# Kernel tuning notes

Hardware: AMD Instinct MI355X
Metric: run time of the kernel (lower is better)

The kernel has to match this reference:

```python
import jax, jax.numpy as jnp
import numpy as np


def setup_inputs() -> dict:
    key = jax.random.key(0)
    ks = jax.random.split(key, 5)
    B, S, E, H = 2, 2048, 1024, 16
    scale = 1.0 / np.sqrt(E)
    return {
        "input": jax.random.normal(ks[0], (B, S, E), dtype=jnp.float32),
        "Wqkv": jax.random.normal(ks[1], (3 * E, E), dtype=jnp.float32) * scale,
        "bqkv": jax.random.normal(ks[2], (3 * E,), dtype=jnp.float32) * 0.01,
        "Wo": jax.random.normal(ks[3], (E, E), dtype=jnp.float32) * scale,
        "bo": jax.random.normal(ks[4], (E,), dtype=jnp.float32) * 0.01,
    }


def reference(input, Wqkv, bqkv, Wo, bo):
    H = 16
    B, S, E = input.shape
    dh = E // H
    # fused QKV projection: [B, S, 3E]
    qkv = input @ Wqkv.T + bqkv
    qkv = qkv.reshape(B, S, 3, H, dh)
    qkv = jnp.transpose(qkv, (2, 0, 3, 1, 4))  # [3, B, H, S, dh]
    q, k, v = qkv[0], qkv[1], qkv[2]
    # scores [B, H, Sq, Sk]
    scores = jnp.einsum("bhqd,bhkd->bhqk", q, k) / jnp.sqrt(jnp.float32(dh))
    # NOTE: original code softmaxes over dim=2 (the QUERY axis) — reproduced faithfully
    attn = jax.nn.softmax(scores, axis=2)
    out = jnp.einsum("bhqk,bhkd->bhqd", attn, v)  # [B, H, S, dh]
    out = jnp.transpose(out, (0, 2, 1, 3)).reshape(B, S, E)
    return out @ Wo.T + bo
```

## Files before the change

kernel.cpp:

```cpp
#include <hip/hip_runtime.h>
#include <math.h>

#define B_ 2
#define S_ 2048
#define E_ 1024
#define H_ 16
#define DH_ 64
#define NE3_ 3072
#define MTOT_ (B_*S_)
#define QSCALE_ 0.18033688011112042f

typedef __bf16 bf16;
typedef bf16 bf16x8 __attribute__((ext_vector_type(8)));
typedef bf16 bf16x4 __attribute__((ext_vector_type(4)));
typedef float f32x4 __attribute__((ext_vector_type(4)));

#define MFMA16(a,b,c) __builtin_amdgcn_mfma_f32_16x16x32_bf16(a,b,c,0,0,0)

#define F_(r) ((((r) & 7) ^ (((r) >> 3) & 7)))

__device__ inline void* lds_swz(void* base, int row, int bytecol) {
    return (char*)base + row * 128 + (bytecol ^ (F_(row) << 4));
}

__device__ inline unsigned cvt_pk_bf16(float lo, float hi) {
    unsigned r;
    asm("v_cvt_pk_bf16_f32 %0, %1, %2" : "=v"(r) : "v"(lo), "v"(hi));
    return r;
}

__device__ inline float exp2_hw(float x) {
    float r;
    asm("v_exp_f32 %0, %1" : "=v"(r) : "v"(x));
    return r;
}

__device__ inline void gload_lds16(const void* g, void* l) {
    __builtin_amdgcn_global_load_lds(
        (const __attribute__((address_space(1))) void*)g,
        (__attribute__((address_space(3))) void*)l, 16, 0, 0);
}

#define NX_ (MTOT_*E_)
#define NW_ (NE3_*E_)
#define NWO_ (E_*E_)
__global__ void k_f2b3(const float* __restrict__ x, const float* __restrict__ wq,
                       const float* __restrict__ wo,
                       bf16* __restrict__ xb, bf16* __restrict__ wqb,
                       bf16* __restrict__ wob) {
    const int i = blockIdx.x * 256 + threadIdx.x;
    const int idx = i * 4;
    const float* src; bf16* dst; int off;
    if (idx < NX_)            { src = x;  dst = xb;  off = idx; }
    else if (idx < NX_ + NW_) { src = wq; dst = wqb; off = idx - NX_; }
    else                      { src = wo; dst = wob; off = idx - NX_ - NW_; }
    float4 f = *reinterpret_cast<const float4*>(src + off);
    bf16x4 o;
    o[0] = (bf16)f.x; o[1] = (bf16)f.y; o[2] = (bf16)f.z; o[3] = (bf16)f.w;
    *reinterpret_cast<bf16x4*>(dst + off) = o;
}

template<int MODE>
__global__ __launch_bounds__(256) void k_gemm(
    const bf16* __restrict__ A, const bf16* __restrict__ W,
    const float* __restrict__ bias,
    bf16* __restrict__ Qb, bf16* __restrict__ Kb, bf16* __restrict__ Vt,
    float* __restrict__ out)
{
    __shared__ __align__(16) bf16 At[2][128*64];
    __shared__ __align__(16) bf16 Bt[2][128*64];
    const int tid = threadIdx.x, lane = tid & 63, w = tid >> 6;
    const int wr = w >> 1, wc = w & 1;
    const int g = blockIdx.x;
    const int nxw = (MODE == 0 ? 3 : 1);
    const int xcd = g & 7, li = g >> 3;
    const int m0 = (li & 31) * 128;
    const int n0 = (xcd * nxw + (li >> 5)) * 128;

    f32x4 acc[4][4] = {};
    const int lrow = lane >> 3, lcol = (lane & 7) * 8;

    auto stage = [&](int k0, int buf) {
        for (int c4 = 0; c4 < 4; ++c4) {
            const int c = w * 4 + c4;
            const int row = c * 8 + lrow;
            const int colx = lcol ^ (F_(row) * 8);
            gload_lds16(A + (size_t)(m0 + row) * E_ + k0 + colx, &At[buf][c * 512]);
            gload_lds16(W + (size_t)(n0 + row) * E_ + k0 + colx, &Bt[buf][c * 512]);
        }
    };
    stage(0, 0);
    __syncthreads();

    int cur = 0;
    for (int kt = 0; kt < E_/64; ++kt) {
        if (kt + 1 < E_/64) stage((kt + 1) * 64, cur ^ 1);
        for (int ks = 0; ks < 2; ++ks) {
            const int bc = ks * 64 + 16 * (lane >> 4);
            bf16x8 a[4], b[4];
            for (int j = 0; j < 4; ++j)
                a[j] = *(const bf16x8*)lds_swz(&At[cur][0], wr*64 + j*16 + (lane&15), bc);
            for (int i = 0; i < 4; ++i)
                b[i] = *(const bf16x8*)lds_swz(&Bt[cur][0], wc*64 + i*16 + (lane&15), bc);
            for (int i = 0; i < 4; ++i)
                for (int j = 0; j < 4; ++j)
                    acc[i][j] = MFMA16(b[i], a[j], acc[i][j]);
        }
        cur ^= 1;
        if (kt + 1 < E_/64) __syncthreads();
    }

    const int mW = m0 + wr*64;
    for (int i = 0; i < 4; ++i) {
        const int n4 = n0 + wc*64 + i*16 + (lane >> 4) * 4;
        const float4 b4 = *reinterpret_cast<const float4*>(&bias[n4]);
        const float* bp = reinterpret_cast<const float*>(&b4);
        if constexpr (MODE == 0) {
            const int t = n4 >> 10, h = (n4 >> 6) & 15, d0 = n4 & 63;
            for (int j = 0; j < 4; ++j) {
                const int m = mW + j*16 + (lane & 15);
                const int bb_i = m >> 11, s = m & 2047;
                if (t == 2) {
                    for (int r = 0; r < 4; ++r)
                        Vt[(((size_t)(bb_i*H_ + h))*DH_ + d0 + r)*S_ + s] =
                            (bf16)(acc[i][j][r] + bp[r]);
                } else {
                    bf16* dst = (t == 0) ? Qb : Kb;
                    const float sc = (t == 0) ? QSCALE_ : 1.0f;
                    bf16x4 o;
                    for (int r = 0; r < 4; ++r)
                        o[r] = (bf16)((acc[i][j][r] + bp[r]) * sc);
                    *reinterpret_cast<bf16x4*>(
                        dst + (((size_t)(bb_i*H_ + h))*S_ + s)*DH_ + d0) = o;
                }
            }
        } else {
            for (int j = 0; j < 4; ++j) {
                const int m = mW + j*16 + (lane & 15);
                float4 o;
                o.x = acc[i][j][0] + bp[0];
                o.y = acc[i][j][1] + bp[1];
                o.z = acc[i][j][2] + bp[2];
                o.w = acc[i][j][3] + bp[3];
                *reinterpret_cast<float4*>(out + (size_t)m * E_ + n4) = o;
            }
        }
    }
}

__global__ __launch_bounds__(256) void k_colsum(
    const bf16* __restrict__ Qb, const bf16* __restrict__ Kb,
    bf16* __restrict__ Vt)
{
    __shared__ __align__(16) bf16 Kl[128*64];
    __shared__ __align__(16) bf16 Ql[2][128*64];
    __shared__ float rlbuf[128];
    const int tid = threadIdx.x, lane = tid & 63, w = tid >> 6;
    const int g = blockIdx.x, xcd = g & 7, li = g >> 3;
    const int bh = xcd * 4 + (li >> 4);
    const int k0 = (li & 15) * 128;
    const bf16* Kbase = Kb + ((size_t)bh * S_ + k0) * DH_;
    const bf16* Qbase = Qb + (size_t)bh * S_ * DH_;

    for (int j = 0; j < 4; ++j) {
        const int idx = j*256 + tid, row = idx >> 3;
        const int colx = ((idx & 7) * 8) ^ (F_(row) * 8);
        gload_lds16(Kbase + (size_t)row * DH_ + colx, &Kl[(j*256 + w*64) * 8]);
    }
    auto stageQ = [&](int qt, int buf) {
        for (int j = 0; j < 4; ++j) {
            const int idx = j*256 + tid, row = idx >> 3;
            const int colx = ((idx & 7) * 8) ^ (F_(row) * 8);
            gload_lds16(Qbase + (size_t)(qt*128 + row) * DH_ + colx,
                        &Ql[buf][(j*256 + w*64) * 8]);
        }
    };
    stageQ(0, 0);
    __syncthreads();

    bf16x8 bk[2][2];
    for (int ks = 0; ks < 2; ++ks) {
        const int bc = ks * 64 + 16 * (lane >> 4);
        bk[ks][0] = *(const bf16x8*)lds_swz(Kl, w*32 + (lane&15), bc);
        bk[ks][1] = *(const bf16x8*)lds_swz(Kl, w*32 + 16 + (lane&15), bc);
    }

    float lsum0 = 0.f, lsum1 = 0.f;
    int cur = 0;
    for (int qt = 0; qt < S_/128; ++qt) {
        if (qt + 1 < S_/128) stageQ(qt + 1, cur ^ 1);
        #pragma unroll
        for (int qi = 0; qi < 8; ++qi) {
            f32x4 s0 = {}, s1 = {};
            for (int ks = 0; ks < 2; ++ks) {
                const int bc = ks * 64 + 16 * (lane >> 4);
                bf16x8 aq = *(const bf16x8*)lds_swz(&Ql[cur][0], qi*16 + (lane&15), bc);
                s0 = MFMA16(aq, bk[ks][0], s0);
                s1 = MFMA16(aq, bk[ks][1], s1);
            }
            for (int r = 0; r < 4; ++r) {
                lsum0 += exp2_hw(s0[r]);
                lsum1 += exp2_hw(s1[r]);
            }
        }
        cur ^= 1;
        if (qt + 1 < S_/128) __syncthreads();
    }
    lsum0 += __shfl_xor(lsum0, 16); lsum0 += __shfl_xor(lsum0, 32);
    lsum1 += __shfl_xor(lsum1, 16); lsum1 += __shfl_xor(lsum1, 32);
    if (lane < 16) {
        rlbuf[w*32 + lane]      = 1.0f / lsum0;
        rlbuf[w*32 + 16 + lane] = 1.0f / lsum1;
    }
    __syncthreads();

    bf16* Vb = Vt + (size_t)bh * DH_ * S_ + k0;
    const int d = tid >> 2, kk = (tid & 3) * 32;
    for (int c = 0; c < 4; ++c) {
        bf16x8* p = reinterpret_cast<bf16x8*>(Vb + (size_t)d * S_ + kk + c*8);
        bf16x8 v = *p, o;
        for (int jj = 0; jj < 8; ++jj)
            o[jj] = (bf16)((float)v[jj] * rlbuf[kk + c*8 + jj]);
        *p = o;
    }
}

__global__ __launch_bounds__(256) void k_attn(
    const bf16* __restrict__ Qb, const bf16* __restrict__ Kb,
    const bf16* __restrict__ Vt, bf16* __restrict__ AO)
{
    __shared__ __align__(16) char smem[49152];
    const int tid = threadIdx.x, lane = tid & 63, w = tid >> 6;
    const int g = blockIdx.x, xcd = g & 7, li = g >> 3;
    const int bh = xcd * 4 + (li >> 4);
    const int q0 = (li & 15) * 128;
    const bf16* Qbase = Qb + ((size_t)bh * S_ + q0) * DH_;
    const bf16* Kbase = Kb + (size_t)bh * S_ * DH_;
    const bf16* Vbase = Vt + (size_t)bh * DH_ * S_;
    char* QP  = smem;
    char* Plw = smem + w * 4096;

    for (int j = 0; j < 4; ++j) {
        const int idx = j*256 + tid, row = idx >> 3;
        const int colx = ((idx & 7) * 8) ^ (F_(row) * 8);
        gload_lds16(Qbase + (size_t)row * DH_ + colx, QP + (j*256 + w*64) * 16);
    }
    auto stageKV = [&](int kt, int buf) {
        for (int j = 0; j < 2; ++j) {
            const int idx = j*256 + tid, row = idx >> 3;
            const int colx = ((idx & 7) * 8) ^ (F_(row) * 8);
            gload_lds16(Kbase + (size_t)(kt*64 + row) * DH_ + colx,
                        smem + 16384 + buf*8192 + (j*256 + w*64) * 16);
            gload_lds16(Vbase + (size_t)row * S_ + kt*64 + colx,
                        smem + 32768 + buf*8192 + (j*256 + w*64) * 16);
        }
    };
    stageKV(0, 0);
    __syncthreads();

    bf16x8 bq[2][2];
    for (int qi = 0; qi < 2; ++qi)
        for (int ks = 0; ks < 2; ++ks)
            bq[qi][ks] = *(const bf16x8*)lds_swz(QP, w*32 + qi*16 + (lane&15),
                                                 ks*64 + 16*(lane>>4));

    f32x4 oacc[4][2] = {};
    int cur = 0;
    for (int kt = 0; kt < S_/64; ++kt) {
        if (kt + 1 < S_/64) stageKV(kt + 1, cur ^ 1);
        char* Kc = smem + 16384 + cur*8192;
        char* Vc = smem + 32768 + cur*8192;

        for (int kf = 0; kf < 4; ++kf) {
            f32x4 sacc[2] = {};
            for (int ks = 0; ks < 2; ++ks) {
                bf16x8 ak = *(const bf16x8*)lds_swz(Kc, kf*16 + (lane&15),
                                                    ks*64 + 16*(lane>>4));
                for (int qi = 0; qi < 2; ++qi)
                    sacc[qi] = MFMA16(ak, bq[qi][ks], sacc[qi]);
            }
            for (int qi = 0; qi < 2; ++qi) {
                uint2 pw;
                pw.x = cvt_pk_bf16(exp2_hw(sacc[qi][0]), exp2_hw(sacc[qi][1]));
                pw.y = cvt_pk_bf16(exp2_hw(sacc[qi][2]), exp2_hw(sacc[qi][3]));
                *(uint2*)lds_swz(Plw, qi*16 + (lane&15), kf*32 + (lane>>4)*8) = pw;
            }
        }

        for (int ks = 0; ks < 2; ++ks) {
            const int bc = ks*64 + 16*(lane>>4);
            bf16x8 av[4], bp[2];
            for (int df = 0; df < 4; ++df)
                av[df] = *(const bf16x8*)lds_swz(Vc, df*16 + (lane&15), bc);
            for (int qi = 0; qi < 2; ++qi)
                bp[qi] = *(const bf16x8*)lds_swz(Plw, qi*16 + (lane&15), bc);
            for (int df = 0; df < 4; ++df)
                for (int qi = 0; qi < 2; ++qi)
                    oacc[df][qi] = MFMA16(av[df], bp[qi], oacc[df][qi]);
        }
        cur ^= 1;
        if (kt + 1 < S_/64) __syncthreads();
    }

    const int b = bh >> 4, h = bh & 15;
    for (int df = 0; df < 4; ++df)
        for (int qi = 0; qi < 2; ++qi) {
            const int d0 = df*16 + (lane >> 4) * 4;
            const int q = q0 + w*32 + qi*16 + (lane & 15);
            bf16x4 o;
            for (int r = 0; r < 4; ++r) o[r] = (bf16)oacc[df][qi][r];
            *reinterpret_cast<bf16x4*>(
                AO + ((size_t)(b*S_ + q))*E_ + h*DH_ + d0) = o;
        }
}

extern "C" void kernel_launch(void* const* d_in, const int* in_sizes, int n_in,
                              void* d_out, int out_size, void* d_ws, size_t ws_size,
                              hipStream_t stream) {
    const float* input = (const float*)d_in[0];
    const float* Wqkv  = (const float*)d_in[1];
    const float* bqkv  = (const float*)d_in[2];
    const float* Wo    = (const float*)d_in[3];
    const float* bo    = (const float*)d_in[4];
    float* out = (float*)d_out;

    char* ws = (char*)d_ws;
    bf16*  Xb   = (bf16*) (ws + 0);
    bf16*  Wqb  = (bf16*) (ws + 8388608);
    bf16*  Wob  = (bf16*) (ws + 14680064);
    bf16*  Qb   = (bf16*) (ws + 16777216);
    bf16*  Kb   = (bf16*) (ws + 25165824);
    bf16*  Vtg  = (bf16*) (ws + 33554432);
    bf16*  AO   = (bf16*) (ws + 41943040);

    k_f2b3<<<(NX_ + NW_ + NWO_) / 1024, 256, 0, stream>>>(
        input, Wqkv, Wo, Xb, Wqb, Wob);

    k_gemm<0><<<768, 256, 0, stream>>>(Xb, Wqb, bqkv, Qb, Kb, Vtg, nullptr);

    k_colsum<<<512, 256, 0, stream>>>(Qb, Kb, Vtg);

    k_attn<<<512, 256, 0, stream>>>(Qb, Kb, Vtg, AO);

    k_gemm<1><<<256, 256, 0, stream>>>(AO, Wob, bo, nullptr, nullptr, nullptr, out);
}
```

Before: 169.2 us.

## Store LDS tiles in MFMA fragment order instead of XOR-swizzled rows

Replaces the XOR-swizzled row-major shared-memory layout with a fragment-major layout. Each 1 KB chunk holds exactly one 16x32 MFMA operand fragment, so every lane reads at a fixed offset of lane*16 with no address arithmetic and no bank conflicts. The global-to-LDS loads are remapped so each wave fills whole fragments, and the P tile in the attention kernel uses a matching layout. The inner loops are also fully unrolled. In exchange, each global load now covers 16 rows by 16 bytes instead of contiguous 128-byte row segments, which can hurt global coalescing.

```diff
diff --git a/kernel.cpp b/kernel.cpp
--- a/kernel.cpp
+++ b/kernel.cpp
@@ -16,12 +16,6 @@
 typedef float f32x4 __attribute__((ext_vector_type(4)));
 
 #define MFMA16(a,b,c) __builtin_amdgcn_mfma_f32_16x16x32_bf16(a,b,c,0,0,0)
-
-#define F_(r) ((((r) & 7) ^ (((r) >> 3) & 7)))
-
-__device__ inline void* lds_swz(void* base, int row, int bytecol) {
-    return (char*)base + row * 128 + (bytecol ^ (F_(row) << 4));
-}
 
 __device__ inline unsigned cvt_pk_bf16(float lo, float hi) {
     unsigned r;
@@ -67,9 +61,12 @@
     bf16* __restrict__ Qb, bf16* __restrict__ Kb, bf16* __restrict__ Vt,
     float* __restrict__ out)
 {
-    __shared__ __align__(16) bf16 At[2][128*64];
-    __shared__ __align__(16) bf16 Bt[2][128*64];
+    __shared__ __align__(16) char smem[65536];
+    char* Abuf = smem;
+    char* Bbuf = smem + 32768;
     const int tid = threadIdx.x, lane = tid & 63, w = tid >> 6;
+    const int lq = lane & 15, lh = lane >> 4;
+    const int l16 = lane * 16;
     const int wr = w >> 1, wc = w & 1;
     const int g = blockIdx.x;
     const int nxw = (MODE == 0 ? 3 : 1);
@@ -77,32 +74,52 @@
     const int m0 = (li & 31) * 128;
     const int n0 = (xcd * nxw + (li >> 5)) * 128;
 
+    const int voffA = lq * E_ + lh * 8;
+
     f32x4 acc[4][4] = {};
-    const int lrow = lane >> 3, lcol = (lane & 7) * 8;
 
     auto stage = [&](int k0, int buf) {
-        for (int c4 = 0; c4 < 4; ++c4) {
-            const int c = w * 4 + c4;
-            const int row = c * 8 + lrow;
-            const int colx = lcol ^ (F_(row) * 8);
-            gload_lds16(A + (size_t)(m0 + row) * E_ + k0 + colx, &At[buf][c * 512]);
-            gload_lds16(W + (size_t)(n0 + row) * E_ + k0 + colx, &Bt[buf][c * 512]);
+        #pragma unroll
+        for (int j = 0; j < 4; ++j) {
+            const int C = j*4 + w;
+            const int rp = (C>>3)*64 + ((C>>1)&3)*16;
+            const int ce = (C&1)*32;
+            gload_lds16(A + (size_t)(m0 + rp) * E_ + k0 + ce + (voffA - lq*E_) + lq*E_,
+                        Abuf + buf*16384 + C*1024);
+            gload_lds16(W + (size_t)(n0 + rp) * E_ + k0 + ce + voffA - lq*E_ + lq*E_,
+                        Bbuf + buf*16384 + C*1024);
         }
     };
-    stage(0, 0);
+    auto stage2 = [&](int k0, int buf) {
+        #pragma unroll
+        for (int j = 0; j < 4; ++j) {
+            const int C = j*4 + w;
+            const int rp = (C>>3)*64 + ((C>>1)&3)*16;
+            const int ce = (C&1)*32;
+            gload_lds16(A + (size_t)(m0 + rp) * E_ + k0 + ce + voffA,
+                        Abuf + buf*16384 + C*1024);
+            gload_lds16(W + (size_t)(n0 + rp) * E_ + k0 + ce + voffA,
+                        Bbuf + buf*16384 + C*1024);
+        }
+    };
+    stage2(0, 0);
     __syncthreads();
 
     int cur = 0;
     for (int kt = 0; kt < E_/64; ++kt) {
-        if (kt + 1 < E_/64) stage((kt + 1) * 64, cur ^ 1);
+        if (kt + 1 < E_/64) stage2((kt + 1) * 64, cur ^ 1);
+        #pragma unroll
         for (int ks = 0; ks < 2; ++ks) {
-            const int bc = ks * 64 + 16 * (lane >> 4);
             bf16x8 a[4], b[4];
+            #pragma unroll
             for (int j = 0; j < 4; ++j)
-                a[j] = *(const bf16x8*)lds_swz(&At[cur][0], wr*64 + j*16 + (lane&15), bc);
+                a[j] = *(const bf16x8*)(Abuf + cur*16384 + (wr*8 + j*2 + ks)*1024 + l16);
+            #pragma unroll
             for (int i = 0; i < 4; ++i)
-                b[i] = *(const bf16x8*)lds_swz(&Bt[cur][0], wc*64 + i*16 + (lane&15), bc);
+                b[i] = *(const bf16x8*)(Bbuf + cur*16384 + (wc*8 + i*2 + ks)*1024 + l16);
+            #pragma unroll
             for (int i = 0; i < 4; ++i)
+                #pragma unroll
                 for (int j = 0; j < 4; ++j)
                     acc[i][j] = MFMA16(b[i], a[j], acc[i][j]);
         }
@@ -112,13 +129,13 @@
 
     const int mW = m0 + wr*64;
     for (int i = 0; i < 4; ++i) {
-        const int n4 = n0 + wc*64 + i*16 + (lane >> 4) * 4;
+        const int n4 = n0 + wc*64 + i*16 + lh * 4;
         const float4 b4 = *reinterpret_cast<const float4*>(&bias[n4]);
         const float* bp = reinterpret_cast<const float*>(&b4);
         if constexpr (MODE == 0) {
             const int t = n4 >> 10, h = (n4 >> 6) & 15, d0 = n4 & 63;
             for (int j = 0; j < 4; ++j) {
-                const int m = mW + j*16 + (lane & 15);
+                const int m = mW + j*16 + lq;
                 const int bb_i = m >> 11, s = m & 2047;
                 if (t == 2) {
                     for (int r = 0; r < 4; ++r)
@@ -136,7 +153,7 @@
             }
         } else {
             for (int j = 0; j < 4; ++j) {
-                const int m = mW + j*16 + (lane & 15);
+                const int m = mW + j*16 + lq;
                 float4 o;
                 o.x = acc[i][j][0] + bp[0];
                 o.y = acc[i][j][1] + bp[1];
@@ -152,38 +169,43 @@
     const bf16* __restrict__ Qb, const bf16* __restrict__ Kb,
     bf16* __restrict__ Vt)
 {
-    __shared__ __align__(16) bf16 Kl[128*64];
-    __shared__ __align__(16) bf16 Ql[2][128*64];
+    __shared__ __align__(16) char smem[49152];
     __shared__ float rlbuf[128];
+    char* Kl   = smem;
+    char* Qbuf = smem + 16384;
     const int tid = threadIdx.x, lane = tid & 63, w = tid >> 6;
+    const int lq = lane & 15, lh = lane >> 4;
+    const int l16 = lane * 16;
     const int g = blockIdx.x, xcd = g & 7, li = g >> 3;
     const int bh = xcd * 4 + (li >> 4);
     const int k0 = (li & 15) * 128;
     const bf16* Kbase = Kb + ((size_t)bh * S_ + k0) * DH_;
     const bf16* Qbase = Qb + (size_t)bh * S_ * DH_;
-
+    const int voffK = lq * DH_ + lh * 8;
+
+    #pragma unroll
     for (int j = 0; j < 4; ++j) {
-        const int idx = j*256 + tid, row = idx >> 3;
-        const int colx = ((idx & 7) * 8) ^ (F_(row) * 8);
-        gload_lds16(Kbase + (size_t)row * DH_ + colx, &Kl[(j*256 + w*64) * 8]);
+        const int C = j*4 + w;
+        const int rp = (C>>2)*32 + ((C>>1)&1)*16;
+        gload_lds16(Kbase + (size_t)rp * DH_ + (C&1)*32 + voffK, Kl + C*1024);
     }
     auto stageQ = [&](int qt, int buf) {
+        #pragma unroll
         for (int j = 0; j < 4; ++j) {
-            const int idx = j*256 + tid, row = idx >> 3;
-            const int colx = ((idx & 7) * 8) ^ (F_(row) * 8);
-            gload_lds16(Qbase + (size_t)(qt*128 + row) * DH_ + colx,
-                        &Ql[buf][(j*256 + w*64) * 8]);
+            const int C = j*4 + w;
+            gload_lds16(Qbase + (size_t)(qt*128 + (C>>1)*16) * DH_ + (C&1)*32 + voffK,
+                        Qbuf + buf*16384 + C*1024);
         }
     };
     stageQ(0, 0);
     __syncthreads();
 
     bf16x8 bk[2][2];
-    for (int ks = 0; ks < 2; ++ks) {
-        const int bc = ks * 64 + 16 * (lane >> 4);
-        bk[ks][0] = *(const bf16x8*)lds_swz(Kl, w*32 + (lane&15), bc);
-        bk[ks][1] = *(const bf16x8*)lds_swz(Kl, w*32 + 16 + (lane&15), bc);
-    }
+    #pragma unroll
+    for (int f = 0; f < 2; ++f)
+        #pragma unroll
+        for (int ks = 0; ks < 2; ++ks)
+            bk[f][ks] = *(const bf16x8*)(Kl + (w*4 + f*2 + ks)*1024 + l16);
 
     float lsum0 = 0.f, lsum1 = 0.f;
     int cur = 0;
@@ -192,12 +214,13 @@
         #pragma unroll
         for (int qi = 0; qi < 8; ++qi) {
             f32x4 s0 = {}, s1 = {};
+            #pragma unroll
             for (int ks = 0; ks < 2; ++ks) {
-                const int bc = ks * 64 + 16 * (lane >> 4);
-                bf16x8 aq = *(const bf16x8*)lds_swz(&Ql[cur][0], qi*16 + (lane&15), bc);
-                s0 = MFMA16(aq, bk[ks][0], s0);
-                s1 = MFMA16(aq, bk[ks][1], s1);
-            }
+                bf16x8 aq = *(const bf16x8*)(Qbuf + cur*16384 + (qi*2+ks)*1024 + l16);
+                s0 = MFMA16(aq, bk[0][ks], s0);
+                s1 = MFMA16(aq, bk[1][ks], s1);
+            }
+            #pragma unroll
             for (int r = 0; r < 4; ++r) {
                 lsum0 += exp2_hw(s0[r]);
                 lsum1 += exp2_hw(s1[r]);
@@ -230,71 +253,87 @@
     const bf16* __restrict__ Vt, bf16* __restrict__ AO)
 {
     __shared__ __align__(16) char smem[49152];
+    char* QP   = smem;
+    char* Kbuf = smem + 16384;
+    char* Vbuf = smem + 32768;
     const int tid = threadIdx.x, lane = tid & 63, w = tid >> 6;
+    const int lq = lane & 15, lh = lane >> 4;
+    const int l16 = lane * 16;
     const int g = blockIdx.x, xcd = g & 7, li = g >> 3;
     const int bh = xcd * 4 + (li >> 4);
     const int q0 = (li & 15) * 128;
     const bf16* Qbase = Qb + ((size_t)bh * S_ + q0) * DH_;
     const bf16* Kbase = Kb + (size_t)bh * S_ * DH_;
     const bf16* Vbase = Vt + (size_t)bh * DH_ * S_;
-    char* QP  = smem;
-    char* Plw = smem + w * 4096;
-
+    char* Plw = QP + w * 4096;
+    const int voffK = lq * DH_ + lh * 8;
+    const int voffV = lq * S_ + lh * 8;
+    const int pOff = (lh >> 1) * 256 + lq * 16 + (lh & 1) * 8;
+
+    #pragma unroll
     for (int j = 0; j < 4; ++j) {
-        const int idx = j*256 + tid, row = idx >> 3;
-        const int colx = ((idx & 7) * 8) ^ (F_(row) * 8);
-        gload_lds16(Qbase + (size_t)row * DH_ + colx, QP + (j*256 + w*64) * 16);
+        const int C = j*4 + w;
+        const int rp = (C>>2)*32 + ((C>>1)&1)*16;
+        gload_lds16(Qbase + (size_t)rp * DH_ + (C&1)*32 + voffK, QP + C*1024);
     }
     auto stageKV = [&](int kt, int buf) {
+        #pragma unroll
         for (int j = 0; j < 2; ++j) {
-            const int idx = j*256 + tid, row = idx >> 3;
-            const int colx = ((idx & 7) * 8) ^ (F_(row) * 8);
-            gload_lds16(Kbase + (size_t)(kt*64 + row) * DH_ + colx,
-                        smem + 16384 + buf*8192 + (j*256 + w*64) * 16);
-            gload_lds16(Vbase + (size_t)row * S_ + kt*64 + colx,
-                        smem + 32768 + buf*8192 + (j*256 + w*64) * 16);
+            const int C = j*4 + w;
+            gload_lds16(Kbase + (size_t)(kt*64 + (C>>1)*16) * DH_ + (C&1)*32 + voffK,
+                        Kbuf + buf*8192 + C*1024);
+            gload_lds16(Vbase + (size_t)((C>>1)*16) * S_ + kt*64 + (C&1)*32 + voffV,
+                        Vbuf + buf*8192 + C*1024);
         }
     };
     stageKV(0, 0);
     __syncthreads();
 
     bf16x8 bq[2][2];
+    #pragma unroll
     for (int qi = 0; qi < 2; ++qi)
+        #pragma unroll
         for (int ks = 0; ks < 2; ++ks)
-            bq[qi][ks] = *(const bf16x8*)lds_swz(QP, w*32 + qi*16 + (lane&15),
-                                                 ks*64 + 16*(lane>>4));
+            bq[qi][ks] = *(const bf16x8*)(QP + w*4096 + (qi*2+ks)*1024 + l16);
 
     f32x4 oacc[4][2] = {};
     int cur = 0;
     for (int kt = 0; kt < S_/64; ++kt) {
         if (kt + 1 < S_/64) stageKV(kt + 1, cur ^ 1);
-        char* Kc = smem + 16384 + cur*8192;
-        char* Vc = smem + 32768 + cur*8192;
-
+        char* Kc = Kbuf + cur*8192;
+        char* Vc = Vbuf + cur*8192;
+
+        #pragma unroll
         for (int kf = 0; kf < 4; ++kf) {
             f32x4 sacc[2] = {};
+            #pragma unroll
             for (int ks = 0; ks < 2; ++ks) {
-                bf16x8 ak = *(const bf16x8*)lds_swz(Kc, kf*16 + (lane&15),
-                                                    ks*64 + 16*(lane>>4));
+                bf16x8 ak = *(const bf16x8*)(Kc + (kf*2+ks)*1024 + l16);
+                #pragma unroll
                 for (int qi = 0; qi < 2; ++qi)
                     sacc[qi] = MFMA16(ak, bq[qi][ks], sacc[qi]);
             }
+            #pragma unroll
             for (int qi = 0; qi < 2; ++qi) {
                 uint2 pw;
                 pw.x = cvt_pk_bf16(exp2_hw(sacc[qi][0]), exp2_hw(sacc[qi][1]));
                 pw.y = cvt_pk_bf16(exp2_hw(sacc[qi][2]), exp2_hw(sacc[qi][3]));
-                *(uint2*)lds_swz(Plw, qi*16 + (lane&15), kf*32 + (lane>>4)*8) = pw;
-            }
-        }
-
+                *(uint2*)(Plw + pOff + (kf>>1)*2048 + (kf&1)*512 + qi*1024) = pw;
+            }
+        }
+
+        #pragma unroll
         for (int ks = 0; ks < 2; ++ks) {
-            const int bc = ks*64 + 16*(lane>>4);
             bf16x8 av[4], bp[2];
+            #pragma unroll
             for (int df = 0; df < 4; ++df)
-                av[df] = *(const bf16x8*)lds_swz(Vc, df*16 + (lane&15), bc);
+                av[df] = *(const bf16x8*)(Vc + (df*2+ks)*1024 + l16);
+            #pragma unroll
             for (int qi = 0; qi < 2; ++qi)
-                bp[qi] = *(const bf16x8*)lds_swz(Plw, qi*16 + (lane&15), bc);
+                bp[qi] = *(const bf16x8*)(Plw + (ks*2+qi)*1024 + l16);
+            #pragma unroll
             for (int df = 0; df < 4; ++df)
+                #pragma unroll
                 for (int qi = 0; qi < 2; ++qi)
                     oacc[df][qi] = MFMA16(av[df], bp[qi], oacc[df][qi]);
         }
@@ -303,10 +342,12 @@
     }
 
     const int b = bh >> 4, h = bh & 15;
+    #pragma unroll
     for (int df = 0; df < 4; ++df)
+        #pragma unroll
         for (int qi = 0; qi < 2; ++qi) {
-            const int d0 = df*16 + (lane >> 4) * 4;
-            const int q = q0 + w*32 + qi*16 + (lane & 15);
+            const int d0 = df*16 + lh * 4;
+            const int q = q0 + w*32 + qi*16 + lq;
             bf16x4 o;
             for (int r = 0; r < 4; ++r) o[r] = (bf16)oacc[df][qi][r];
             *reinterpret_cast<bf16x4*>(
```

After: 187.9 us. 11.1% more time.
